# Optimization experiments

Measured on AMD Instinct MI355X. Metric: run time of the kernel, lower is better.

## Reference

```python
import jax, jax.numpy as jnp
import numpy as np

B, C, L = 4, 256, 4096
C8 = C // 8

def setup_inputs() -> dict:
    key = jax.random.key(0)
    ks = jax.random.split(key, 8)
    s = 1.0 / np.sqrt(C)
    x = jax.random.normal(ks[0], (B, C, L), dtype=jnp.float32)
    Wq = jax.random.normal(ks[1], (C8, C), dtype=jnp.float32) * s
    bq = jax.random.normal(ks[2], (C8,), dtype=jnp.float32) * s
    Wk = jax.random.normal(ks[3], (C8, C), dtype=jnp.float32) * s
    bk = jax.random.normal(ks[4], (C8,), dtype=jnp.float32) * s
    Wv = jax.random.normal(ks[5], (C, C), dtype=jnp.float32) * s
    bv = jax.random.normal(ks[6], (C,), dtype=jnp.float32) * s
    gamma = jax.random.normal(ks[7], (1,), dtype=jnp.float32) * 0.1
    return {"x": x, "Wq": Wq, "bq": bq, "Wk": Wk, "bk": bk, "Wv": Wv, "bv": bv, "gamma": gamma}

def reference(x, Wq, bq, Wk, bk, Wv, bv, gamma):
    # pointwise conv1d == channel matmul: [O,C] x [B,C,L] -> [B,O,L]
    q = jnp.einsum('oc,bcl->bol', Wq, x) + bq[None, :, None]   # [B, C8, L]
    k = jnp.einsum('oc,bcl->bol', Wk, x) + bk[None, :, None]   # [B, C8, L]
    v = jnp.einsum('oc,bcl->bol', Wv, x) + bv[None, :, None]   # [B, C,  L]
    # attention[b,i,j] = sum_c q[b,c,i] * k[b,c,j]
    attn = jnp.einsum('bci,bcj->bij', q, k)                    # [B, L, L]
    attn = jax.nn.softmax(attn, axis=-1)
    # out[b,c,i] = sum_j v[b,c,j] * attn[b,i,j]
    out = jnp.einsum('bcj,bij->bci', v, attn)                  # [B, C, L]
    return gamma * out + x
```

## Files before the change

kernel.cpp:

```cpp
#include <hip/hip_runtime.h>
#include <math.h>

#define BB 4
#define CC 256
#define LL 4096
#define DD 32
#define LOG2E 1.44269504088896f

typedef __attribute__((ext_vector_type(8))) short short8;
typedef __attribute__((ext_vector_type(4))) short short4v;
typedef __attribute__((ext_vector_type(4))) float f32x4;
typedef __attribute__((ext_vector_type(4))) unsigned int uint4v;
typedef __attribute__((ext_vector_type(2))) unsigned int uint2v;

#define BARRIER() asm volatile("s_waitcnt lgkmcnt(0)\n\ts_barrier" ::: "memory")

__device__ inline unsigned short f2bf(float f) {
  union { float f; unsigned u; } v; v.f = f;
  unsigned r = v.u + 0x7fffu + ((v.u >> 16) & 1u);
  return (unsigned short)(r >> 16);
}

__device__ inline float fast_exp2(float x) {
#if __has_builtin(__builtin_amdgcn_exp2f)
  return __builtin_amdgcn_exp2f(x);
#else
  return exp2f(x);
#endif
}

__device__ __host__ inline int sigma32(int p) {
  const int q4 = (p >> 3) & 3, u = p & 7;
  return 16 * (u >> 2) + 4 * q4 + (u & 3);
}

__global__ __launch_bounds__(256) void wprep_kernel(
    const float* __restrict__ Wq, const float* __restrict__ Wk, const float* __restrict__ Wv,
    unsigned short* __restrict__ wf)
{
  const int t = threadIdx.x;
  const int ot = blockIdx.x >> 1;
  const int rep = blockIdx.x & 1;
  const int lane = t & 63, cl = lane & 15, q4 = lane >> 4;
  const int ks = (t >> 6) + 4 * rep;
  const int o = ot * 16 + cl;
  const int c = ks * 32 + q4 * 8;
  const float* src = (o < 32) ? (Wq + o * CC) : (o < 64) ? (Wk + (o - 32) * CC)
                                              : (Wv + (o - 64) * CC);
  const float sc = (o < 32) ? LOG2E : 1.0f;
  unsigned short p[8];
  #pragma unroll
  for (int j = 0; j < 8; ++j) p[j] = f2bf(src[c + j] * sc);
  uint4v u;
  u.x = (unsigned)p[0] | ((unsigned)p[1] << 16);
  u.y = (unsigned)p[2] | ((unsigned)p[3] << 16);
  u.z = (unsigned)p[4] | ((unsigned)p[5] << 16);
  u.w = (unsigned)p[6] | ((unsigned)p[7] << 16);
  *(uint4v*)(wf + ((size_t)(ot * 8 + ks) * 64 + lane) * 8) = u;
}

__global__ __launch_bounds__(512, 4) void qkv_kernel(
    const float* __restrict__ x, const unsigned short* __restrict__ wf,
    const float* __restrict__ bq, const float* __restrict__ bk, const float* __restrict__ bv,
    unsigned short* __restrict__ qT, unsigned short* __restrict__ kT,
    unsigned short* __restrict__ vf)
{
  __shared__ union {
    float xl[32 * 261];
    struct {
      unsigned short qk[32 * 72];
      __align__(16) unsigned short v[256 * 40];
    } ep;
  } sm;

  const int t = threadIdx.x;
  const int lane = t & 63, cl = lane & 15, q4 = lane >> 4;
  const int blk = blockIdx.x;
  const int b  = (blk & 7) >> 1;
  const int it = ((blk >> 3) << 1) + (blk & 1);
  const int i0 = it * 32;

  {
    const int ln8 = t & 7;
    #pragma unroll
    for (int p = 0; p < 4; ++p) {
      const int c = (t >> 3) + 64 * p;
      const f32x4 v = *(const f32x4*)(x + ((size_t)(b * CC + c)) * LL + i0 + ln8 * 4);
      #pragma unroll
      for (int k = 0; k < 4; ++k) sm.xl[(ln8 * 4 + k) * 261 + c] = v[k];
    }
  }
  __syncthreads();

  const int wi = (t >> 6) & 1, wo = t >> 7;
  const f32x4 zero = {0.f, 0.f, 0.f, 0.f};
  f32x4 acc[5];
  #pragma unroll
  for (int u = 0; u < 5; ++u) acc[u] = zero;

  for (int ks = 0; ks < 8; ++ks) {
    unsigned short p[8];
    #pragma unroll
    for (int j = 0; j < 8; ++j)
      p[j] = f2bf(sm.xl[(16 * wi + cl) * 261 + ks * 32 + q4 * 8 + j]);
    union { short8 s; uint4v u; } bfr;
    bfr.u.x = (unsigned)p[0] | ((unsigned)p[1] << 16);
    bfr.u.y = (unsigned)p[2] | ((unsigned)p[3] << 16);
    bfr.u.z = (unsigned)p[4] | ((unsigned)p[5] << 16);
    bfr.u.w = (unsigned)p[6] | ((unsigned)p[7] << 16);
    #pragma unroll
    for (int u = 0; u < 5; ++u) {
      const short8 a = *(const short8*)(wf + ((size_t)((wo * 5 + u) * 8 + ks) * 64 + lane) * 8);
      acc[u] = __builtin_amdgcn_mfma_f32_16x16x32_bf16(a, bfr.s, acc[u], 0, 0, 0);
    }
  }
  __syncthreads();

  #pragma unroll
  for (int u = 0; u < 5; ++u) {
    const int g = wo * 5 + u;
    if (g < 4) {
      short4v pk;
      #pragma unroll
      for (int r = 0; r < 4; ++r) {
        const int o = 16 * g + 4 * q4 + r;
        const float v = acc[u][r] + ((o < 32) ? bq[o] * LOG2E : bk[o - 32]);
        pk[r] = (short)f2bf(v);
      }
      *(short4v*)&sm.ep.qk[(16 * wi + cl) * 72 + 16 * g + 4 * q4] = pk;
    } else {
      #pragma unroll
      for (int r = 0; r < 4; ++r) {
        const int ch = 16 * (g - 4) + 4 * q4 + r;
        sm.ep.v[ch * 40 + 16 * wi + cl] = f2bf(acc[u][r] + bv[ch]);
      }
    }
  }
  __syncthreads();

  if (t < 64) {
    const int i = t >> 1, which = t & 1;
    const int gi = i0 + i;
    const unsigned short* srcp = &sm.ep.qk[i * 72 + which * 32];
    uint4v d0 = *(const uint4v*)(srcp + 0);
    uint4v d1 = *(const uint4v*)(srcp + 8);
    uint4v d2 = *(const uint4v*)(srcp + 16);
    uint4v d3 = *(const uint4v*)(srcp + 24);
    unsigned short* dst;
    if (which == 0) {
      dst = qT + ((size_t)b * LL + gi) * DD;
    } else {
      const int row = (gi & ~31) + sigma32(gi & 31);
      dst = kT + ((size_t)b * LL + row) * DD;
    }
    *(uint4v*)dst = d0; *(uint4v*)(dst + 8) = d1;
    *(uint4v*)(dst + 16) = d2; *(uint4v*)(dst + 24) = d3;
  }
  const int kk = it & 1, jt = it >> 1;
  #pragma unroll
  for (int rep = 0; rep < 2; ++rep) {
    const int slot = t + 512 * rep;
    const int fl = slot >> 6, l2 = slot & 63;
    const int cl2 = l2 & 15, q42 = l2 >> 4;
    const int m4 = fl >> 2, mt = fl & 3;
    const int fg = 8 * m4 + 4 * kk + mt;
    const int ch = 64 * m4 + 16 * mt + cl2;
    const uint4v d = *(const uint4v*)&sm.ep.v[ch * 40 + q42 * 8];
    *(uint4v*)(vf + (((size_t)(b * 64 + jt)) * 32 + fg) * 512 + l2 * 8) = d;
  }
}

__global__ __launch_bounds__(1024, 4) void attn_kernel(
    const unsigned short* __restrict__ qT, const unsigned short* __restrict__ kT,
    const unsigned short* __restrict__ vf, const float* __restrict__ x,
    const float* __restrict__ gamma_p, float* __restrict__ out)
{
  __shared__ union {
    unsigned short P[2][8][4][2][64][4];
    float Om[8][8][64][4];
  } sm;
  __shared__ float l_buf[16][64];

  const int t = threadIdx.x;
  const int w = t >> 6, lane = t & 63, cl = lane & 15, q4 = lane >> 4;
  const int m8 = w >> 1, kh = w & 1;
  const int blk = blockIdx.x;
  const int b  = (blk & 7) >> 1;
  const int it = ((blk >> 3) << 1) + (blk & 1);
  const int i0 = it * 64;

  short8 qa[4];
  #pragma unroll
  for (int nt = 0; nt < 4; ++nt)
    qa[nt] = *(const short8*)(qT + ((size_t)b * LL + i0 + 16 * nt + cl) * DD + q4 * 8);

  const f32x4 zero = {0.f, 0.f, 0.f, 0.f};
  f32x4 O[2][4];
  #pragma unroll
  for (int mtp = 0; mtp < 2; ++mtp)
    #pragma unroll
    for (int nt = 0; nt < 4; ++nt) O[mtp][nt] = zero;
  float l_r[4] = {0.f, 0.f, 0.f, 0.f};

  const unsigned short* kbase = kT + ((size_t)b * LL + 16 * w + cl) * DD + q4 * 8;
  const unsigned short* vroot = vf + ((size_t)(b * 64)) * 32 * 512 + lane * 8;
  const int mtg = 2 * (m8 & 1), m4b = 8 * (m8 >> 1);

  short8 kb = *(const short8*)kbase;
  short8 va[2][2];
  #pragma unroll
  for (int e = 0; e < 2; ++e) {
    const int kk = kh * 4 + e;
    const int fg = m4b + 4 * (kk & 1) + mtg;
    #pragma unroll
    for (int mtp = 0; mtp < 2; ++mtp)
      va[e][mtp] = *(const short8*)(vroot + ((size_t)((kk >> 1) * 32) + fg + mtp) * 512);
  }

  for (int ss = 0; ss < 16; ++ss) {
    const int buf = ss & 1;

    f32x4 s[4];
    #pragma unroll
    for (int nt = 0; nt < 4; ++nt)
      s[nt] = __builtin_amdgcn_mfma_f32_16x16x32_bf16(kb, qa[nt], zero, 0, 0, 0);
    kb = *(const short8*)(kbase + (size_t)((ss + 1) & 15) * 256 * DD);

    #pragma unroll
    for (int nt = 0; nt < 4; ++nt) {
      const float e0 = fast_exp2(s[nt][0]);
      const float e1 = fast_exp2(s[nt][1]);
      const float e2 = fast_exp2(s[nt][2]);
      const float e3 = fast_exp2(s[nt][3]);
      uint2v uv;
      uv.x = __builtin_amdgcn_perm(__float_as_uint(e1), __float_as_uint(e0), 0x07060302);
      uv.y = __builtin_amdgcn_perm(__float_as_uint(e3), __float_as_uint(e2), 0x07060302);
      *(uint2v*)&sm.P[buf][w >> 1][nt][w & 1][lane][0] = uv;
      float sum = (e0 + e1) + (e2 + e3);
      sum += __shfl_xor(sum, 16);
      sum += __shfl_xor(sum, 32);
      l_r[nt] += sum;
    }
    BARRIER();

    #pragma unroll
    for (int e = 0; e < 4; ++e) {
      const int kk = kh * 4 + e;
      short8 pb[4];
      #pragma unroll
      for (int nt = 0; nt < 4; ++nt) {
        union { short8 s8; uint2v h[2]; } pbu;
        pbu.h[0] = *(const uint2v*)&sm.P[buf][kk][nt][0][lane][0];
        pbu.h[1] = *(const uint2v*)&sm.P[buf][kk][nt][1][lane][0];
        pb[nt] = pbu.s8;
      }
      #pragma unroll
      for (int nt = 0; nt < 4; ++nt) {
        O[0][nt] = __builtin_amdgcn_mfma_f32_16x16x32_bf16(va[e & 1][0], pb[nt], O[0][nt], 0, 0, 0);
        O[1][nt] = __builtin_amdgcn_mfma_f32_16x16x32_bf16(va[e & 1][1], pb[nt], O[1][nt], 0, 0, 0);
      }
      const int nss = (e < 2) ? ss : ((ss + 1) & 15);
      const int nkk = (e < 2) ? (kk + 2) : (kh * 4 + (e - 2));
      const int fg = m4b + 4 * (nkk & 1) + mtg;
      const size_t base = ((size_t)(nss * 4 + (nkk >> 1)) * 32 + fg) * 512;
      #pragma unroll
      for (int mtp = 0; mtp < 2; ++mtp)
        va[e & 1][mtp] = *(const short8*)(vroot + base + mtp * 512);
    }
  }

  if (lane < 16) {
    #pragma unroll
    for (int nt = 0; nt < 4; ++nt) l_buf[w][16 * nt + lane] = l_r[nt];
  }
  BARRIER();
  if (kh == 1) {
    #pragma unroll
    for (int mtp = 0; mtp < 2; ++mtp)
      #pragma unroll
      for (int nt = 0; nt < 4; ++nt)
        *(f32x4*)&sm.Om[m8][mtp * 4 + nt][lane][0] = O[mtp][nt];
  }
  BARRIER();
  if (kh == 0) {
    const float gam = gamma_p[0];
    float inv_l[4];
    #pragma unroll
    for (int nt = 0; nt < 4; ++nt) {
      float s = 0.f;
      #pragma unroll
      for (int sl = 0; sl < 16; ++sl) s += l_buf[sl][16 * nt + cl];
      inv_l[nt] = 1.0f / s;
    }
    #pragma unroll
    for (int mtp = 0; mtp < 2; ++mtp) {
      #pragma unroll
      for (int nt = 0; nt < 4; ++nt) {
        const f32x4 om = *(const f32x4*)&sm.Om[m8][mtp * 4 + nt][lane][0];
        #pragma unroll
        for (int r = 0; r < 4; ++r) {
          const int ch = 32 * m8 + 16 * mtp + 4 * q4 + r;
          const int i  = i0 + 16 * nt + cl;
          const size_t idx = ((size_t)b * CC + ch) * LL + i;
          out[idx] = gam * (O[mtp][nt][r] + om[r]) * inv_l[nt] + x[idx];
        }
      }
    }
  }
}

extern "C" void kernel_launch(void* const* d_in, const int* in_sizes, int n_in,
                              void* d_out, int out_size, void* d_ws, size_t ws_size,
                              hipStream_t stream) {
  const float* x     = (const float*)d_in[0];
  const float* Wq    = (const float*)d_in[1];
  const float* bq    = (const float*)d_in[2];
  const float* Wk    = (const float*)d_in[3];
  const float* bk    = (const float*)d_in[4];
  const float* Wv    = (const float*)d_in[5];
  const float* bv    = (const float*)d_in[6];
  const float* gamma = (const float*)d_in[7];
  float* out = (float*)d_out;

  unsigned short* qT = (unsigned short*)d_ws;
  unsigned short* kT = qT + (size_t)BB * LL * DD;
  unsigned short* vf = kT + (size_t)BB * LL * DD;
  unsigned short* wf = (unsigned short*)d_out;

  wprep_kernel<<<40, 256, 0, stream>>>(Wq, Wk, Wv, wf);
  qkv_kernel<<<512, 512, 0, stream>>>(x, wf, bq, bk, bv, qT, kT, vf);
  attn_kernel<<<256, 1024, 0, stream>>>(qT, kT, vf, x, gamma, out);
}
```

Measured before the change: 143.4 us.

## Halve attention block query tile and rebalance per-wave K/V work split

Attention blocks now handle 32 query rows with 8 waves instead of 64 rows with 16 waves, launching twice as many blocks. Each wave computes two key sub-tiles for scores and four channel tiles for the PV product, and row-sum reduction moves from shuffles to an LDS epilogue reduction. The intent is better CU occupancy and load balance, at the cost of doubling K/V re-reads across blocks and more accumulator registers per wave.

Measured after the change: 141.5 us. About the same (-1.4%).

```diff
diff --git a/kernel.cpp b/kernel.cpp
--- a/kernel.cpp
+++ b/kernel.cpp
@@ -170,139 +170,146 @@
   }
 }
 
-__global__ __launch_bounds__(1024, 4) void attn_kernel(
+__global__ __launch_bounds__(512, 4) void attn_kernel(
     const unsigned short* __restrict__ qT, const unsigned short* __restrict__ kT,
     const unsigned short* __restrict__ vf, const float* __restrict__ x,
     const float* __restrict__ gamma_p, float* __restrict__ out)
 {
   __shared__ union {
-    unsigned short P[2][8][4][2][64][4];
-    float Om[8][8][64][4];
+    unsigned short P[2][8][2][2][64][4];
+    float Om[4][8][64][4];
   } sm;
-  __shared__ float l_buf[16][64];
+  __shared__ float l_lds[8][2][64];
 
   const int t = threadIdx.x;
   const int w = t >> 6, lane = t & 63, cl = lane & 15, q4 = lane >> 4;
-  const int m8 = w >> 1, kh = w & 1;
+  const int m4 = w & 3, kh = w >> 2;
   const int blk = blockIdx.x;
   const int b  = (blk & 7) >> 1;
   const int it = ((blk >> 3) << 1) + (blk & 1);
-  const int i0 = it * 64;
-
-  short8 qa[4];
-  #pragma unroll
-  for (int nt = 0; nt < 4; ++nt)
+  const int i0 = it * 32;
+
+  short8 qa[2];
+  #pragma unroll
+  for (int nt = 0; nt < 2; ++nt)
     qa[nt] = *(const short8*)(qT + ((size_t)b * LL + i0 + 16 * nt + cl) * DD + q4 * 8);
 
   const f32x4 zero = {0.f, 0.f, 0.f, 0.f};
-  f32x4 O[2][4];
-  #pragma unroll
-  for (int mtp = 0; mtp < 2; ++mtp)
-    #pragma unroll
-    for (int nt = 0; nt < 4; ++nt) O[mtp][nt] = zero;
-  float l_r[4] = {0.f, 0.f, 0.f, 0.f};
-
-  const unsigned short* kbase = kT + ((size_t)b * LL + 16 * w + cl) * DD + q4 * 8;
+  f32x4 O[4][2];
+  #pragma unroll
+  for (int mt = 0; mt < 4; ++mt)
+    #pragma unroll
+    for (int nt = 0; nt < 2; ++nt) O[mt][nt] = zero;
+  float l_r[2] = {0.f, 0.f};
+
+  const unsigned short* kbase = kT + ((size_t)b * LL + 32 * w + cl) * DD + q4 * 8;
   const unsigned short* vroot = vf + ((size_t)(b * 64)) * 32 * 512 + lane * 8;
-  const int mtg = 2 * (m8 & 1), m4b = 8 * (m8 >> 1);
-
-  short8 kb = *(const short8*)kbase;
-  short8 va[2][2];
+
+  short8 kb[2];
+  #pragma unroll
+  for (int h = 0; h < 2; ++h)
+    kb[h] = *(const short8*)(kbase + (size_t)(16 * h) * DD);
+
+  short8 va[2][4];
   #pragma unroll
   for (int e = 0; e < 2; ++e) {
-    const int kk = kh * 4 + e;
-    const int fg = m4b + 4 * (kk & 1) + mtg;
-    #pragma unroll
-    for (int mtp = 0; mtp < 2; ++mtp)
-      va[e][mtp] = *(const short8*)(vroot + ((size_t)((kk >> 1) * 32) + fg + mtp) * 512);
+    const int kk = 4 * kh + e;
+    const size_t base = ((size_t)((kk >> 1) * 32) + 8 * m4 + 4 * (kk & 1)) * 512;
+    #pragma unroll
+    for (int mt = 0; mt < 4; ++mt)
+      va[e][mt] = *(const short8*)(vroot + base + mt * 512);
   }
 
   for (int ss = 0; ss < 16; ++ss) {
     const int buf = ss & 1;
 
-    f32x4 s[4];
-    #pragma unroll
-    for (int nt = 0; nt < 4; ++nt)
-      s[nt] = __builtin_amdgcn_mfma_f32_16x16x32_bf16(kb, qa[nt], zero, 0, 0, 0);
-    kb = *(const short8*)(kbase + (size_t)((ss + 1) & 15) * 256 * DD);
-
-    #pragma unroll
-    for (int nt = 0; nt < 4; ++nt) {
-      const float e0 = fast_exp2(s[nt][0]);
-      const float e1 = fast_exp2(s[nt][1]);
-      const float e2 = fast_exp2(s[nt][2]);
-      const float e3 = fast_exp2(s[nt][3]);
-      uint2v uv;
-      uv.x = __builtin_amdgcn_perm(__float_as_uint(e1), __float_as_uint(e0), 0x07060302);
-      uv.y = __builtin_amdgcn_perm(__float_as_uint(e3), __float_as_uint(e2), 0x07060302);
-      *(uint2v*)&sm.P[buf][w >> 1][nt][w & 1][lane][0] = uv;
-      float sum = (e0 + e1) + (e2 + e3);
-      sum += __shfl_xor(sum, 16);
-      sum += __shfl_xor(sum, 32);
-      l_r[nt] += sum;
-    }
+    f32x4 s[2][2];
+    #pragma unroll
+    for (int h = 0; h < 2; ++h)
+      #pragma unroll
+      for (int nt = 0; nt < 2; ++nt)
+        s[h][nt] = __builtin_amdgcn_mfma_f32_16x16x32_bf16(kb[h], qa[nt], zero, 0, 0, 0);
+    #pragma unroll
+    for (int h = 0; h < 2; ++h)
+      kb[h] = *(const short8*)(kbase + (size_t)(((ss + 1) & 15) * 256 + 16 * h) * DD);
+
+    #pragma unroll
+    for (int h = 0; h < 2; ++h)
+      #pragma unroll
+      for (int nt = 0; nt < 2; ++nt) {
+        const float e0 = fast_exp2(s[h][nt][0]);
+        const float e1 = fast_exp2(s[h][nt][1]);
+        const float e2 = fast_exp2(s[h][nt][2]);
+        const float e3 = fast_exp2(s[h][nt][3]);
+        uint2v uv;
+        uv.x = __builtin_amdgcn_perm(__float_as_uint(e1), __float_as_uint(e0), 0x07060302);
+        uv.y = __builtin_amdgcn_perm(__float_as_uint(e3), __float_as_uint(e2), 0x07060302);
+        *(uint2v*)&sm.P[buf][w][nt][h][lane][0] = uv;
+        l_r[nt] += (e0 + e1) + (e2 + e3);
+      }
     BARRIER();
 
     #pragma unroll
     for (int e = 0; e < 4; ++e) {
-      const int kk = kh * 4 + e;
-      short8 pb[4];
-      #pragma unroll
-      for (int nt = 0; nt < 4; ++nt) {
+      const int kk = 4 * kh + e;
+      short8 pb[2];
+      #pragma unroll
+      for (int nt = 0; nt < 2; ++nt) {
         union { short8 s8; uint2v h[2]; } pbu;
         pbu.h[0] = *(const uint2v*)&sm.P[buf][kk][nt][0][lane][0];
         pbu.h[1] = *(const uint2v*)&sm.P[buf][kk][nt][1][lane][0];
         pb[nt] = pbu.s8;
       }
       #pragma unroll
-      for (int nt = 0; nt < 4; ++nt) {
-        O[0][nt] = __builtin_amdgcn_mfma_f32_16x16x32_bf16(va[e & 1][0], pb[nt], O[0][nt], 0, 0, 0);
-        O[1][nt] = __builtin_amdgcn_mfma_f32_16x16x32_bf16(va[e & 1][1], pb[nt], O[1][nt], 0, 0, 0);
-      }
+      for (int mt = 0; mt < 4; ++mt)
+        #pragma unroll
+        for (int nt = 0; nt < 2; ++nt)
+          O[mt][nt] = __builtin_amdgcn_mfma_f32_16x16x32_bf16(va[e & 1][mt], pb[nt],
+                                                              O[mt][nt], 0, 0, 0);
       const int nss = (e < 2) ? ss : ((ss + 1) & 15);
-      const int nkk = (e < 2) ? (kk + 2) : (kh * 4 + (e - 2));
-      const int fg = m4b + 4 * (nkk & 1) + mtg;
-      const size_t base = ((size_t)(nss * 4 + (nkk >> 1)) * 32 + fg) * 512;
-      #pragma unroll
-      for (int mtp = 0; mtp < 2; ++mtp)
-        va[e & 1][mtp] = *(const short8*)(vroot + base + mtp * 512);
-    }
-  }
-
-  if (lane < 16) {
-    #pragma unroll
-    for (int nt = 0; nt < 4; ++nt) l_buf[w][16 * nt + lane] = l_r[nt];
-  }
+      const int nkk = (e < 2) ? (kk + 2) : (4 * kh + (e - 2));
+      const size_t base = ((size_t)(nss * 4 + (nkk >> 1)) * 32 + 8 * m4 + 4 * (nkk & 1)) * 512;
+      #pragma unroll
+      for (int mt = 0; mt < 4; ++mt)
+        va[e & 1][mt] = *(const short8*)(vroot + base + mt * 512);
+    }
+  }
+
+  l_lds[w][0][lane] = l_r[0];
+  l_lds[w][1][lane] = l_r[1];
   BARRIER();
   if (kh == 1) {
     #pragma unroll
-    for (int mtp = 0; mtp < 2; ++mtp)
-      #pragma unroll
-      for (int nt = 0; nt < 4; ++nt)
-        *(f32x4*)&sm.Om[m8][mtp * 4 + nt][lane][0] = O[mtp][nt];
+    for (int mt = 0; mt < 4; ++mt)
+      #pragma unroll
+      for (int nt = 0; nt < 2; ++nt)
+        *(f32x4*)&sm.Om[m4][mt * 2 + nt][lane][0] = O[mt][nt];
   }
   BARRIER();
   if (kh == 0) {
     const float gam = gamma_p[0];
-    float inv_l[4];
-    #pragma unroll
-    for (int nt = 0; nt < 4; ++nt) {
+    float inv_l[2];
+    #pragma unroll
+    for (int nt = 0; nt < 2; ++nt) {
       float s = 0.f;
       #pragma unroll
-      for (int sl = 0; sl < 16; ++sl) s += l_buf[sl][16 * nt + cl];
+      for (int sl = 0; sl < 8; ++sl)
+        #pragma unroll
+        for (int g = 0; g < 4; ++g)
+          s += l_lds[sl][nt][g * 16 + cl];
       inv_l[nt] = 1.0f / s;
     }
     #pragma unroll
-    for (int mtp = 0; mtp < 2; ++mtp) {
-      #pragma unroll
-      for (int nt = 0; nt < 4; ++nt) {
-        const f32x4 om = *(const f32x4*)&sm.Om[m8][mtp * 4 + nt][lane][0];
+    for (int mt = 0; mt < 4; ++mt) {
+      #pragma unroll
+      for (int nt = 0; nt < 2; ++nt) {
+        const f32x4 om = *(const f32x4*)&sm.Om[m4][mt * 2 + nt][lane][0];
         #pragma unroll
         for (int r = 0; r < 4; ++r) {
-          const int ch = 32 * m8 + 16 * mtp + 4 * q4 + r;
+          const int ch = 64 * m4 + 16 * mt + 4 * q4 + r;
           const int i  = i0 + 16 * nt + cl;
           const size_t idx = ((size_t)b * CC + ch) * LL + i;
-          out[idx] = gam * (O[mtp][nt][r] + om[r]) * inv_l[nt] + x[idx];
+          out[idx] = gam * (O[mt][nt][r] + om[r]) * inv_l[nt] + x[idx];
         }
       }
     }
@@ -329,5 +336,5 @@
 
   wprep_kernel<<<40, 256, 0, stream>>>(Wq, Wk, Wv, wf);
   qkv_kernel<<<512, 512, 0, stream>>>(x, wf, bq, bk, bv, qT, kT, vf);
-  attn_kernel<<<256, 1024, 0, stream>>>(qT, kT, vf, x, gamma, out);
-}
+  attn_kernel<<<512, 512, 0, stream>>>(qT, kT, vf, x, gamma, out);
+}
```
